# Kernel tuning notes

Hardware: AMD Instinct MI355X
Metric: run time of the kernel (lower is better)

The kernel has to match this reference:

```python
import jax, jax.numpy as jnp
import numpy as np

B, N, C = 4, 2048, 768
H = 12
D = C // H  # 64
HID = 4 * C  # 3072
EPS = 1e-5


def layer_norm(x, g, b):
    mu = jnp.mean(x, axis=-1, keepdims=True)
    var = jnp.mean(jnp.square(x - mu), axis=-1, keepdims=True)
    return (x - mu) * jax.lax.rsqrt(var + EPS) * g + b


def setup_inputs() -> dict:
    key = jax.random.key(0)
    ks = jax.random.split(key, 12)
    s = lambda fan_in: 1.0 / np.sqrt(fan_in)
    return {
        "x": jax.random.normal(ks[0], (B, N, C), jnp.float32),
        "ln1_g": jnp.ones((C,), jnp.float32),
        "ln1_b": jnp.zeros((C,), jnp.float32),
        "qkv_w": jax.random.normal(ks[1], (3 * C, C), jnp.float32) * s(C),
        "proj_w": jax.random.normal(ks[2], (C, C), jnp.float32) * s(C),
        "proj_b": jnp.zeros((C,), jnp.float32),
        "ln2_g": jnp.ones((C,), jnp.float32),
        "ln2_b": jnp.zeros((C,), jnp.float32),
        "fc1_w": jax.random.normal(ks[3], (HID, C), jnp.float32) * s(C),
        "fc1_b": jnp.zeros((HID,), jnp.float32),
        "fc2_w": jax.random.normal(ks[4], (C, HID), jnp.float32) * s(HID),
        "fc2_b": jnp.zeros((C,), jnp.float32),
    }


def reference(x, ln1_g, ln1_b, qkv_w, proj_w, proj_b, ln2_g, ln2_b, fc1_w, fc1_b, fc2_w, fc2_b):
    # ---- attention branch ----
    h = layer_norm(x, ln1_g, ln1_b)
    qkv = jnp.einsum('bnc,fc->bnf', h, qkv_w)            # [B,N,3C]
    qkv = qkv.reshape(B, N, 3, H, D)
    q, k, v = jnp.moveaxis(qkv, 2, 0)                     # each [B,N,H,D]
    q = jnp.transpose(q, (0, 2, 1, 3)) * (D ** -0.5)      # [B,H,N,D]
    k = jnp.transpose(k, (0, 2, 1, 3))
    v = jnp.transpose(v, (0, 2, 1, 3))
    attn = jax.nn.softmax(jnp.einsum('bhnd,bhmd->bhnm', q, k), axis=-1)
    o = jnp.einsum('bhnm,bhmd->bhnd', attn, v)            # [B,H,N,D]
    o = jnp.transpose(o, (0, 2, 1, 3)).reshape(B, N, C)
    o = jnp.einsum('bnc,oc->bno', o, proj_w) + proj_b
    x = x + o
    # ---- MLP branch ----
    h = layer_norm(x, ln2_g, ln2_b)
    h = jnp.einsum('bnc,hc->bnh', h, fc1_w) + fc1_b
    h = jax.nn.gelu(h, approximate=False)
    h = jnp.einsum('bnh,ch->bnc', h, fc2_w) + fc2_b
    return x + h
```

## Files before the change

kernel.cpp:

```cpp
#include <hip/hip_runtime.h>
#include <math.h>

typedef __bf16 bf16;
typedef __bf16 bf16x4 __attribute__((ext_vector_type(4)));
typedef __bf16 bf16x8 __attribute__((ext_vector_type(8)));
typedef float  f32x4  __attribute__((ext_vector_type(4)));

#define B_   4
#define N_   2048
#define C_   768
#define H_   12
#define T_   8192
#define HID_ 3072

typedef const __attribute__((address_space(1))) unsigned int* as1_u32;
typedef __attribute__((address_space(3))) unsigned int* as3_u32;
__device__ __forceinline__ void gl_lds16(const void* g, void* l) {
    __builtin_amdgcn_global_load_lds((as1_u32)g, (as3_u32)l, 16, 0, 0);
}

__global__ __launch_bounds__(256)
void ln_kernel(const float* __restrict__ inp, const float* __restrict__ g,
               const float* __restrict__ bsh, bf16* __restrict__ out)
{
    int wave = threadIdx.x >> 6, lane = threadIdx.x & 63;
    long long row = (long long)blockIdx.x * 4 + wave;
    const float* p = inp + row * C_;
    float v[12];
    #pragma unroll
    for (int i = 0; i < 12; i++) v[i] = p[i * 64 + lane];
    float s = 0.f, s2 = 0.f;
    #pragma unroll
    for (int i = 0; i < 12; i++) { s += v[i]; s2 += v[i] * v[i]; }
    #pragma unroll
    for (int m = 1; m < 64; m <<= 1) {
        s  += __shfl_xor(s,  m, 64);
        s2 += __shfl_xor(s2, m, 64);
    }
    float mu  = s  * (1.f / C_);
    float var = s2 * (1.f / C_) - mu * mu;
    float rs  = rsqrtf(var + 1e-5f);
    bf16* o = out + row * C_;
    #pragma unroll
    for (int i = 0; i < 12; i++) {
        int c = i * 64 + lane;
        o[c] = (bf16)(((v[i] - mu) * rs) * g[c] + bsh[c]);
    }
}

template<int MODE>
__global__ __launch_bounds__(256)
void gemm_bt(const bf16* __restrict__ A, const float* __restrict__ Bw,
             int M, int N, int K,
             const float* __restrict__ bias,
             void* out, bf16* out2)
{
    __shared__ bf16 At[128 * 32];
    __shared__ bf16 Bt[128 * 32];
    int tid  = threadIdx.x;
    int lane = tid & 63, wave = tid >> 6;
    int quad = lane >> 4, l15 = lane & 15;
    int bm = blockIdx.x, bn = blockIdx.y;
    int wm = wave >> 1, wn = wave & 1;
    int swz = (l15 >> 1) & 3;

    f32x4 acc[4][4];
    f32x4 zero = {0.f, 0.f, 0.f, 0.f};
    #pragma unroll
    for (int mt = 0; mt < 4; mt++)
        #pragma unroll
        for (int nt = 0; nt < 4; nt++) acc[mt][nt] = zero;

    int arow = tid >> 2;
    int aq   = (tid & 3) ^ ((arow >> 1) & 3);
    const bf16*  ag = A  + (size_t)(bm * 128 + arow) * K + aq * 8;
    const float* bg = Bw + (size_t)(bn * 128 + arow) * K + aq * 8;

    for (int k0 = 0; k0 < K; k0 += 32) {
        gl_lds16(ag,                    &At[tid * 8]);
        gl_lds16(ag + (size_t)64 * K,   &At[2048 + tid * 8]);
        f32x4 b0a = *(const f32x4*)(bg);
        f32x4 b0b = *(const f32x4*)(bg + 4);
        f32x4 b1a = *(const f32x4*)(bg + (size_t)64 * K);
        f32x4 b1b = *(const f32x4*)(bg + (size_t)64 * K + 4);
        bf16x8 b0, b1;
        #pragma unroll
        for (int j = 0; j < 4; j++) {
            b0[j] = (bf16)b0a[j]; b0[4 + j] = (bf16)b0b[j];
            b1[j] = (bf16)b1a[j]; b1[4 + j] = (bf16)b1b[j];
        }
        *(bf16x8*)(&Bt[tid * 8])        = b0;
        *(bf16x8*)(&Bt[2048 + tid * 8]) = b1;
        ag += 32; bg += 32;
        __syncthreads();

        bf16x8 af[4], bfr[4];
        #pragma unroll
        for (int mt = 0; mt < 4; mt++)
            af[mt] = *(const bf16x8*)(&At[wm * 2048 + (mt * 16 + l15) * 32 + ((quad ^ swz) << 3)]);
        #pragma unroll
        for (int nt = 0; nt < 4; nt++)
            bfr[nt] = *(const bf16x8*)(&Bt[wn * 2048 + (nt * 16 + l15) * 32 + ((quad ^ swz) << 3)]);
        #pragma unroll
        for (int mt = 0; mt < 4; mt++)
            #pragma unroll
            for (int nt = 0; nt < 4; nt++)
                acc[mt][nt] = __builtin_amdgcn_mfma_f32_16x16x32_bf16(
                    af[mt], bfr[nt], acc[mt][nt], 0, 0, 0);
        __syncthreads();
    }

    if (MODE == 3) {
        if (bn < 12) {
            #pragma unroll
            for (int nt = 0; nt < 4; nt++) {
                int col = bn * 128 + wn * 64 + nt * 16 + l15;
                #pragma unroll
                for (int mt = 0; mt < 4; mt++)
                    #pragma unroll
                    for (int r = 0; r < 4; r++) {
                        int row = bm * 128 + wm * 64 + mt * 16 + quad * 4 + r;
                        ((bf16*)out)[(size_t)row * 1536 + col] = (bf16)acc[mt][nt][r];
                    }
            }
        } else {
            int b = bm >> 4;
            #pragma unroll
            for (int nt = 0; nt < 4; nt++) {
                int vcol = bn * 128 - 1536 + wn * 64 + nt * 16 + l15;
                int h = vcol >> 6, d = vcol & 63;
                size_t rowbase = ((size_t)(b * H_ + h) * 64 + d) * N_;
                #pragma unroll
                for (int mt = 0; mt < 4; mt++) {
                    int n0 = (bm & 15) * 128 + wm * 64 + mt * 16 + quad * 4;
                    bf16x4 pv;
                    #pragma unroll
                    for (int r = 0; r < 4; r++) pv[r] = (bf16)acc[mt][nt][r];
                    *(bf16x4*)(&out2[rowbase + n0]) = pv;
                }
            }
        }
    } else {
        #pragma unroll
        for (int nt = 0; nt < 4; nt++) {
            int col = bn * 128 + wn * 64 + nt * 16 + l15;
            float bv = bias[col];
            #pragma unroll
            for (int mt = 0; mt < 4; mt++) {
                #pragma unroll
                for (int r = 0; r < 4; r++) {
                    int row = bm * 128 + wm * 64 + mt * 16 + quad * 4 + r;
                    size_t idx = (size_t)row * N + col;
                    float v = acc[mt][nt][r] + bv;
                    float ge = 0.5f * v * (1.f + erff(v * 0.70710678118f));
                    ((bf16*)out)[idx] = (bf16)ge;
                }
            }
        }
    }
}

__global__ __launch_bounds__(256)
void gemm64(const bf16* __restrict__ A, const float* __restrict__ Bw,
            int K, const float* __restrict__ bias,
            const float* resid_f, float* out)
{
    __shared__ bf16 At[2][128 * 32];
    __shared__ bf16 Bt[2][64 * 32];
    int tid  = threadIdx.x;
    int lane = tid & 63, wave = tid >> 6;
    int quad = lane >> 4, l15 = lane & 15;
    int bm = blockIdx.x, bn = blockIdx.y;
    int wm = wave >> 1, wn = wave & 1;
    int swz = (l15 >> 1) & 3;

    f32x4 acc[4][2];
    f32x4 zero = {0.f, 0.f, 0.f, 0.f};
    #pragma unroll
    for (int mt = 0; mt < 4; mt++)
        #pragma unroll
        for (int nt = 0; nt < 2; nt++) acc[mt][nt] = zero;

    int arow = tid >> 2;
    int aq   = (tid & 3) ^ ((arow >> 1) & 3);
    const bf16*  ag = A  + (size_t)(bm * 128 + arow) * K + aq * 8;
    const float* bg = Bw + (size_t)(bn * 64  + arow) * K + aq * 8;

    {
        gl_lds16(ag,                  &At[0][tid * 8]);
        gl_lds16(ag + (size_t)64 * K, &At[0][2048 + tid * 8]);
        f32x4 ba = *(const f32x4*)(bg);
        f32x4 bb = *(const f32x4*)(bg + 4);
        bf16x8 b0;
        #pragma unroll
        for (int j = 0; j < 4; j++) { b0[j] = (bf16)ba[j]; b0[4 + j] = (bf16)bb[j]; }
        *(bf16x8*)(&Bt[0][tid * 8]) = b0;
    }
    __syncthreads();

    int nk = K >> 5;
    for (int kt = 0; kt < nk; kt++) {
        int cur = kt & 1, nxt = cur ^ 1;
        if (kt + 1 < nk) {
            const bf16*  agn = ag + (size_t)(kt + 1) * 32;
            const float* bgn = bg + (size_t)(kt + 1) * 32;
            gl_lds16(agn,                  &At[nxt][tid * 8]);
            gl_lds16(agn + (size_t)64 * K, &At[nxt][2048 + tid * 8]);
            f32x4 ba = *(const f32x4*)(bgn);
            f32x4 bb = *(const f32x4*)(bgn + 4);
            bf16x8 b0;
            #pragma unroll
            for (int j = 0; j < 4; j++) { b0[j] = (bf16)ba[j]; b0[4 + j] = (bf16)bb[j]; }
            *(bf16x8*)(&Bt[nxt][tid * 8]) = b0;
        }
        bf16x8 af[4], bfr[2];
        #pragma unroll
        for (int mt = 0; mt < 4; mt++)
            af[mt] = *(const bf16x8*)(&At[cur][wm * 2048 + (mt * 16 + l15) * 32 + ((quad ^ swz) << 3)]);
        #pragma unroll
        for (int nt = 0; nt < 2; nt++)
            bfr[nt] = *(const bf16x8*)(&Bt[cur][(wn * 32 + nt * 16 + l15) * 32 + ((quad ^ swz) << 3)]);
        #pragma unroll
        for (int mt = 0; mt < 4; mt++)
            #pragma unroll
            for (int nt = 0; nt < 2; nt++)
                acc[mt][nt] = __builtin_amdgcn_mfma_f32_16x16x32_bf16(
                    af[mt], bfr[nt], acc[mt][nt], 0, 0, 0);
        __syncthreads();
    }

    #pragma unroll
    for (int nt = 0; nt < 2; nt++) {
        int col = bn * 64 + wn * 32 + nt * 16 + l15;
        float bv = bias[col];
        #pragma unroll
        for (int mt = 0; mt < 4; mt++) {
            #pragma unroll
            for (int r = 0; r < 4; r++) {
                int row = bm * 128 + wm * 64 + mt * 16 + quad * 4 + r;
                size_t idx = (size_t)row * C_ + col;
                out[idx] = acc[mt][nt][r] + bv + resid_f[idx];
            }
        }
    }
}

__global__ __launch_bounds__(256)
void attn_kernel(const bf16* __restrict__ qk, const bf16* __restrict__ vt,
                 bf16* __restrict__ o)
{
    __shared__ bf16 Kt[2][64 * 64];
    __shared__ bf16 Vt[2][64 * 64];
    __shared__ bf16 Pt[4][2][16 * 64];

    int tid = threadIdx.x, lane = tid & 63, wave = tid >> 6;
    int quad = lane >> 4, l15 = lane & 15;
    int swz = (l15 & 7);
    int blk = blockIdx.x;
    int qb = blk & 15;
    int bh = blk >> 4;
    int b = bh / H_, h = bh % H_;

    const bf16* qbase = qk + (size_t)(b * N_) * 1536 + h * 64;
    const bf16* kbase = qbase + 768;
    const bf16* vtb   = vt + (size_t)(bh * 64) * N_;

    bf16x8 qf[2][2];
    #pragma unroll
    for (int qi = 0; qi < 2; qi++) {
        int q = qb * 128 + wave * 32 + qi * 16 + l15;
        const bf16* qp = qbase + (size_t)q * 1536 + quad * 8;
        qf[qi][0] = *(const bf16x8*)(qp);
        qf[qi][1] = *(const bf16x8*)(qp + 32);
    }

    int srow = tid >> 3, schk = tid & 7;
    int soA = srow * 64 + ((schk ^ (srow & 7)) << 3);
    int soB = (srow + 32) * 64 + ((schk ^ (srow & 7)) << 3);

    bf16x8 kr0, kr1, vr0, vr1;
    const bf16* kg0 = kbase + (size_t)srow * 1536 + schk * 8;
    const bf16* vg0 = vtb + (size_t)srow * N_ + schk * 8;

    {
        kr0 = *(const bf16x8*)(kg0);
        kr1 = *(const bf16x8*)(kg0 + (size_t)32 * 1536);
        vr0 = *(const bf16x8*)(vg0);
        vr1 = *(const bf16x8*)(vg0 + (size_t)32 * N_);
        *(bf16x8*)(&Kt[0][soA]) = kr0;  *(bf16x8*)(&Kt[0][soB]) = kr1;
        *(bf16x8*)(&Vt[0][soA]) = vr0;  *(bf16x8*)(&Vt[0][soB]) = vr1;
    }
    __syncthreads();

    f32x4 oacc[2][4];
    f32x4 zero = {0.f, 0.f, 0.f, 0.f};
    #pragma unroll
    for (int qi = 0; qi < 2; qi++)
        #pragma unroll
        for (int nt = 0; nt < 4; nt++) oacc[qi][nt] = zero;
    float mrun[2] = {-1e30f, -1e30f}, lrun[2] = {0.f, 0.f};

    for (int kt = 0; kt < 32; kt++) {
        int cur = kt & 1;
        if (kt < 31) {
            const bf16* kg = kg0 + (size_t)(kt + 1) * 64 * 1536;
            const bf16* vg = vg0 + (size_t)(kt + 1) * 64;
            kr0 = *(const bf16x8*)(kg);
            kr1 = *(const bf16x8*)(kg + (size_t)32 * 1536);
            vr0 = *(const bf16x8*)(vg);
            vr1 = *(const bf16x8*)(vg + (size_t)32 * N_);
        }
        const bf16* KtC = &Kt[cur][0];
        const bf16* VtC = &Vt[cur][0];

        #pragma unroll
        for (int qi = 0; qi < 2; qi++) {
            f32x4 s[4];
            #pragma unroll
            for (int nt = 0; nt < 4; nt++) {
                const bf16* krow = KtC + (nt * 16 + l15) * 64;
                bf16x8 ka0 = *(const bf16x8*)(krow + ((quad ^ swz) << 3));
                bf16x8 ka1 = *(const bf16x8*)(krow + (((4 + quad) ^ swz) << 3));
                f32x4 sv = zero;
                sv = __builtin_amdgcn_mfma_f32_16x16x32_bf16(ka0, qf[qi][0], sv, 0, 0, 0);
                sv = __builtin_amdgcn_mfma_f32_16x16x32_bf16(ka1, qf[qi][1], sv, 0, 0, 0);
                s[nt] = sv;
            }
            float mx = -1e30f;
            #pragma unroll
            for (int nt = 0; nt < 4; nt++)
                #pragma unroll
                for (int r = 0; r < 4; r++) mx = fmaxf(mx, s[nt][r]);
            mx = fmaxf(mx, __shfl_xor(mx, 16, 64));
            mx = fmaxf(mx, __shfl_xor(mx, 32, 64));
            float mnew = fmaxf(mrun[qi], mx * 0.125f);
            float al   = __expf(mrun[qi] - mnew);
            mrun[qi] = mnew;
            float ps = 0.f;
            #pragma unroll
            for (int nt = 0; nt < 4; nt++)
                #pragma unroll
                for (int r = 0; r < 4; r++) {
                    float pv = __expf(s[nt][r] * 0.125f - mnew);
                    s[nt][r] = pv;
                    ps += pv;
                }
            ps += __shfl_xor(ps, 16, 64);
            ps += __shfl_xor(ps, 32, 64);
            lrun[qi] = lrun[qi] * al + ps;
            #pragma unroll
            for (int nt = 0; nt < 4; nt++) oacc[qi][nt] *= al;
            bf16* pw = &Pt[wave][qi][0];
            #pragma unroll
            for (int nt = 0; nt < 4; nt++) {
                bf16x4 pk;
                #pragma unroll
                for (int r = 0; r < 4; r++) pk[r] = (bf16)s[nt][r];
                int ofs = l15 * 64 + (((nt * 2 + (quad >> 1)) ^ swz) << 3) + ((quad & 1) << 2);
                *(bf16x4*)(&pw[ofs]) = pk;
            }
        }

        #pragma unroll
        for (int kc = 0; kc < 2; kc++) {
            int pofs = l15 * 64 + (((kc * 4 + quad) ^ swz) << 3);
            bf16x8 pb0 = *(const bf16x8*)(&Pt[wave][0][pofs]);
            bf16x8 pb1 = *(const bf16x8*)(&Pt[wave][1][pofs]);
            #pragma unroll
            for (int nt = 0; nt < 4; nt++) {
                bf16x8 va = *(const bf16x8*)(VtC + (nt * 16 + l15) * 64 +
                                             (((kc * 4 + quad) ^ swz) << 3));
                oacc[0][nt] = __builtin_amdgcn_mfma_f32_16x16x32_bf16(va, pb0, oacc[0][nt], 0, 0, 0);
                oacc[1][nt] = __builtin_amdgcn_mfma_f32_16x16x32_bf16(va, pb1, oacc[1][nt], 0, 0, 0);
            }
        }

        if (kt < 31) {
            int nxt = cur ^ 1;
            *(bf16x8*)(&Kt[nxt][soA]) = kr0;  *(bf16x8*)(&Kt[nxt][soB]) = kr1;
            *(bf16x8*)(&Vt[nxt][soA]) = vr0;  *(bf16x8*)(&Vt[nxt][soB]) = vr1;
        }
        __syncthreads();
    }

    #pragma unroll
    for (int qi = 0; qi < 2; qi++) {
        int q = qb * 128 + wave * 32 + qi * 16 + l15;
        float inv = 1.f / lrun[qi];
        bf16* ob = o + (size_t)(b * N_ + q) * C_ + h * 64 + quad * 4;
        #pragma unroll
        for (int nt = 0; nt < 4; nt++) {
            bf16x4 pk;
            #pragma unroll
            for (int r = 0; r < 4; r++) pk[r] = (bf16)(oacc[qi][nt][r] * inv);
            *(bf16x4*)(&ob[nt * 16]) = pk;
        }
    }
}

extern "C" void kernel_launch(void* const* d_in, const int* in_sizes, int n_in,
                              void* d_out, int out_size, void* d_ws, size_t ws_size,
                              hipStream_t stream)
{
    const float* x      = (const float*)d_in[0];
    const float* ln1_g  = (const float*)d_in[1];
    const float* ln1_b  = (const float*)d_in[2];
    const float* qkv_w  = (const float*)d_in[3];
    const float* proj_w = (const float*)d_in[4];
    const float* proj_b = (const float*)d_in[5];
    const float* ln2_g  = (const float*)d_in[6];
    const float* ln2_b  = (const float*)d_in[7];
    const float* fc1_w  = (const float*)d_in[8];
    const float* fc1_b  = (const float*)d_in[9];
    const float* fc2_w  = (const float*)d_in[10];
    const float* fc2_b  = (const float*)d_in[11];
    float* out = (float*)d_out;

    char* ws = (char*)d_ws;
    bf16* QK = (bf16*)ws;
    bf16* VT = (bf16*)(ws + (size_t)T_ * 1536 * 2);
    bf16* G  = (bf16*)ws;
    bf16* R1 = (bf16*)(ws + (size_t)T_ * HID_ * 2);

    ln_kernel<<<T_ / 4, 256, 0, stream>>>(x, ln1_g, ln1_b, R1);
    gemm_bt<3><<<dim3(T_ / 128, 2304 / 128), 256, 0, stream>>>(
        R1, qkv_w, T_, 2304, C_, nullptr, QK, VT);
    attn_kernel<<<48 * 16, 256, 0, stream>>>(QK, VT, R1);
    gemm64<<<dim3(T_ / 128, C_ / 64), 256, 0, stream>>>(
        R1, proj_w, C_, proj_b, x, out);
    ln_kernel<<<T_ / 4, 256, 0, stream>>>(out, ln2_g, ln2_b, R1);
    gemm_bt<2><<<dim3(T_ / 128, HID_ / 128), 256, 0, stream>>>(
        R1, fc1_w, T_, HID_, C_, fc1_b, G, nullptr);
    gemm64<<<dim3(T_ / 128, C_ / 64), 256, 0, stream>>>(
        G, fc2_w, HID_, fc2_b, out, out);
}
```

Before: 527.0 us.

## Double-buffer gemm_bt LDS tiles and defer B conversion past MFMA

Adds LDS double buffering to the main gemm_bt kernel, so the next K-tile's A (async global-to-LDS) and B (fp32 register loads) are issued before the current tile's MFMAs. In both GEMM kernels the fp32-to-bf16 conversion and LDS store of B are moved after the MFMA block, so global load latency is hidden behind compute rather than stalling before it. The cost is doubled shared memory in gemm_bt and extra live registers for the prefetched B values, which may lower occupancy.

```diff
diff --git a/kernel.cpp b/kernel.cpp
--- a/kernel.cpp
+++ b/kernel.cpp
@@ -55,8 +55,8 @@
              const float* __restrict__ bias,
              void* out, bf16* out2)
 {
-    __shared__ bf16 At[128 * 32];
-    __shared__ bf16 Bt[128 * 32];
+    __shared__ bf16 At[2][128 * 32];
+    __shared__ bf16 Bt[2][128 * 32];
     int tid  = threadIdx.x;
     int lane = tid & 63, wave = tid >> 6;
     int quad = lane >> 4, l15 = lane & 15;
@@ -73,40 +73,66 @@
 
     int arow = tid >> 2;
     int aq   = (tid & 3) ^ ((arow >> 1) & 3);
-    const bf16*  ag = A  + (size_t)(bm * 128 + arow) * K + aq * 8;
-    const float* bg = Bw + (size_t)(bn * 128 + arow) * K + aq * 8;
-
-    for (int k0 = 0; k0 < K; k0 += 32) {
-        gl_lds16(ag,                    &At[tid * 8]);
-        gl_lds16(ag + (size_t)64 * K,   &At[2048 + tid * 8]);
-        f32x4 b0a = *(const f32x4*)(bg);
-        f32x4 b0b = *(const f32x4*)(bg + 4);
-        f32x4 b1a = *(const f32x4*)(bg + (size_t)64 * K);
-        f32x4 b1b = *(const f32x4*)(bg + (size_t)64 * K + 4);
+    const bf16*  ag0 = A  + (size_t)(bm * 128 + arow) * K + aq * 8;
+    const float* bg0 = Bw + (size_t)(bn * 128 + arow) * K + aq * 8;
+
+    gl_lds16(ag0,                    &At[0][tid * 8]);
+    gl_lds16(ag0 + (size_t)64 * K,   &At[0][2048 + tid * 8]);
+    {
+        f32x4 b0a = *(const f32x4*)(bg0);
+        f32x4 b0b = *(const f32x4*)(bg0 + 4);
+        f32x4 b1a = *(const f32x4*)(bg0 + (size_t)64 * K);
+        f32x4 b1b = *(const f32x4*)(bg0 + (size_t)64 * K + 4);
         bf16x8 b0, b1;
         #pragma unroll
         for (int j = 0; j < 4; j++) {
             b0[j] = (bf16)b0a[j]; b0[4 + j] = (bf16)b0b[j];
             b1[j] = (bf16)b1a[j]; b1[4 + j] = (bf16)b1b[j];
         }
-        *(bf16x8*)(&Bt[tid * 8])        = b0;
-        *(bf16x8*)(&Bt[2048 + tid * 8]) = b1;
-        ag += 32; bg += 32;
-        __syncthreads();
+        *(bf16x8*)(&Bt[0][tid * 8])        = b0;
+        *(bf16x8*)(&Bt[0][2048 + tid * 8]) = b1;
+    }
+    __syncthreads();
+
+    int nk = K >> 5;
+    f32x4 pba, pbb, pca, pcb;
+    for (int kt = 0; kt < nk; kt++) {
+        int cur = kt & 1, nxt = cur ^ 1;
+        if (kt + 1 < nk) {
+            const bf16*  ag = ag0 + (size_t)(kt + 1) * 32;
+            const float* bg = bg0 + (size_t)(kt + 1) * 32;
+            gl_lds16(ag,                  &At[nxt][tid * 8]);
+            gl_lds16(ag + (size_t)64 * K, &At[nxt][2048 + tid * 8]);
+            pba = *(const f32x4*)(bg);
+            pbb = *(const f32x4*)(bg + 4);
+            pca = *(const f32x4*)(bg + (size_t)64 * K);
+            pcb = *(const f32x4*)(bg + (size_t)64 * K + 4);
+        }
 
         bf16x8 af[4], bfr[4];
         #pragma unroll
         for (int mt = 0; mt < 4; mt++)
-            af[mt] = *(const bf16x8*)(&At[wm * 2048 + (mt * 16 + l15) * 32 + ((quad ^ swz) << 3)]);
+            af[mt] = *(const bf16x8*)(&At[cur][wm * 2048 + (mt * 16 + l15) * 32 + ((quad ^ swz) << 3)]);
         #pragma unroll
         for (int nt = 0; nt < 4; nt++)
-            bfr[nt] = *(const bf16x8*)(&Bt[wn * 2048 + (nt * 16 + l15) * 32 + ((quad ^ swz) << 3)]);
+            bfr[nt] = *(const bf16x8*)(&Bt[cur][wn * 2048 + (nt * 16 + l15) * 32 + ((quad ^ swz) << 3)]);
         #pragma unroll
         for (int mt = 0; mt < 4; mt++)
             #pragma unroll
             for (int nt = 0; nt < 4; nt++)
                 acc[mt][nt] = __builtin_amdgcn_mfma_f32_16x16x32_bf16(
                     af[mt], bfr[nt], acc[mt][nt], 0, 0, 0);
+
+        if (kt + 1 < nk) {
+            bf16x8 b0, b1;
+            #pragma unroll
+            for (int j = 0; j < 4; j++) {
+                b0[j] = (bf16)pba[j]; b0[4 + j] = (bf16)pbb[j];
+                b1[j] = (bf16)pca[j]; b1[4 + j] = (bf16)pcb[j];
+            }
+            *(bf16x8*)(&Bt[nxt][tid * 8])        = b0;
+            *(bf16x8*)(&Bt[nxt][2048 + tid * 8]) = b1;
+        }
         __syncthreads();
     }
 
@@ -183,14 +209,14 @@
 
     int arow = tid >> 2;
     int aq   = (tid & 3) ^ ((arow >> 1) & 3);
-    const bf16*  ag = A  + (size_t)(bm * 128 + arow) * K + aq * 8;
-    const float* bg = Bw + (size_t)(bn * 64  + arow) * K + aq * 8;
-
+    const bf16*  ag0 = A  + (size_t)(bm * 128 + arow) * K + aq * 8;
+    const float* bg0 = Bw + (size_t)(bn * 64  + arow) * K + aq * 8;
+
+    gl_lds16(ag0,                  &At[0][tid * 8]);
+    gl_lds16(ag0 + (size_t)64 * K, &At[0][2048 + tid * 8]);
     {
-        gl_lds16(ag,                  &At[0][tid * 8]);
-        gl_lds16(ag + (size_t)64 * K, &At[0][2048 + tid * 8]);
-        f32x4 ba = *(const f32x4*)(bg);
-        f32x4 bb = *(const f32x4*)(bg + 4);
+        f32x4 ba = *(const f32x4*)(bg0);
+        f32x4 bb = *(const f32x4*)(bg0 + 4);
         bf16x8 b0;
         #pragma unroll
         for (int j = 0; j < 4; j++) { b0[j] = (bf16)ba[j]; b0[4 + j] = (bf16)bb[j]; }
@@ -199,20 +225,18 @@
     __syncthreads();
 
     int nk = K >> 5;
+    f32x4 pba, pbb;
     for (int kt = 0; kt < nk; kt++) {
         int cur = kt & 1, nxt = cur ^ 1;
         if (kt + 1 < nk) {
-            const bf16*  agn = ag + (size_t)(kt + 1) * 32;
-            const float* bgn = bg + (size_t)(kt + 1) * 32;
-            gl_lds16(agn,                  &At[nxt][tid * 8]);
-            gl_lds16(agn + (size_t)64 * K, &At[nxt][2048 + tid * 8]);
-            f32x4 ba = *(const f32x4*)(bgn);
-            f32x4 bb = *(const f32x4*)(bgn + 4);
-            bf16x8 b0;
-            #pragma unroll
-            for (int j = 0; j < 4; j++) { b0[j] = (bf16)ba[j]; b0[4 + j] = (bf16)bb[j]; }
-            *(bf16x8*)(&Bt[nxt][tid * 8]) = b0;
-        }
+            const bf16*  ag = ag0 + (size_t)(kt + 1) * 32;
+            const float* bg = bg0 + (size_t)(kt + 1) * 32;
+            gl_lds16(ag,                  &At[nxt][tid * 8]);
+            gl_lds16(ag + (size_t)64 * K, &At[nxt][2048 + tid * 8]);
+            pba = *(const f32x4*)(bg);
+            pbb = *(const f32x4*)(bg + 4);
+        }
+
         bf16x8 af[4], bfr[2];
         #pragma unroll
         for (int mt = 0; mt < 4; mt++)
@@ -226,6 +250,13 @@
             for (int nt = 0; nt < 2; nt++)
                 acc[mt][nt] = __builtin_amdgcn_mfma_f32_16x16x32_bf16(
                     af[mt], bfr[nt], acc[mt][nt], 0, 0, 0);
+
+        if (kt + 1 < nk) {
+            bf16x8 b0;
+            #pragma unroll
+            for (int j = 0; j < 4; j++) { b0[j] = (bf16)pba[j]; b0[4 + j] = (bf16)pbb[j]; }
+            *(bf16x8*)(&Bt[nxt][tid * 8]) = b0;
+        }
         __syncthreads();
     }
 
```

Measured after the change: 495.6 us. 1.06x faster.
